# Performance work log

Measured on AMD Instinct MI355X. Metric: run time of the kernel, lower is better.

The kernel has to match this reference:

```python
import jax, jax.numpy as jnp
import numpy as np

B, S, E = 8, 1024, 512
H = 8            # num_heads
D = E // H       # head_dim
FFN = 2048
WINDOW = 5       # local_window_size
EPS = 1e-5


def _mha(x, in_w, in_b, out_w, out_b, mask=None):
    """PyTorch nn.MultiheadAttention (batch_first) forward. mask: True = blocked."""
    b, s, e = x.shape
    qkv = x @ in_w.T + in_b                      # [B,S,3E]
    q, k, v = jnp.split(qkv, 3, axis=-1)
    def heads(t):
        return t.reshape(b, s, H, D).transpose(0, 2, 1, 3)  # [B,H,S,D]
    q, k, v = heads(q), heads(k), heads(v)
    scores = jnp.einsum('bhsd,bhtd->bhst', q, k) / np.sqrt(D).astype(x.dtype)
    if mask is not None:
        scores = jnp.where(mask[None, None], -jnp.inf, scores)
    attn = jax.nn.softmax(scores, axis=-1)
    out = jnp.einsum('bhst,bhtd->bhsd', attn, v)  # [B,H,S,D]
    out = out.transpose(0, 2, 1, 3).reshape(b, s, e)
    return out @ out_w.T + out_b


def _layernorm(x, g, b):
    mu = jnp.mean(x, axis=-1, keepdims=True)
    var = jnp.mean(jnp.square(x - mu), axis=-1, keepdims=True)
    return (x - mu) * jax.lax.rsqrt(var + EPS) * g + b


def setup_inputs() -> dict:
    key = jax.random.key(0)
    ks = jax.random.split(key, 8)
    w = 0.02  # weight scale for numerical sanity
    return {
        'x': jax.random.normal(ks[0], (B, S, E), jnp.float32),
        'l_in_w': jax.random.normal(ks[1], (3 * E, E), jnp.float32) * w,
        'l_in_b': jnp.zeros((3 * E,), jnp.float32),
        'l_out_w': jax.random.normal(ks[2], (E, E), jnp.float32) * w,
        'l_out_b': jnp.zeros((E,), jnp.float32),
        'g_in_w': jax.random.normal(ks[3], (3 * E, E), jnp.float32) * w,
        'g_in_b': jnp.zeros((3 * E,), jnp.float32),
        'g_out_w': jax.random.normal(ks[4], (E, E), jnp.float32) * w,
        'g_out_b': jnp.zeros((E,), jnp.float32),
        'ffn_w1': jax.random.normal(ks[5], (FFN, E), jnp.float32) * w,
        'ffn_b1': jnp.zeros((FFN,), jnp.float32),
        'ffn_w2': jax.random.normal(ks[6], (E, FFN), jnp.float32) * w,
        'ffn_b2': jnp.zeros((E,), jnp.float32),
        'ln1_g': jnp.ones((E,), jnp.float32),
        'ln1_b': jnp.zeros((E,), jnp.float32),
        'ln2_g': jnp.ones((E,), jnp.float32),
        'ln2_b': jnp.zeros((E,), jnp.float32),
    }


def reference(x, l_in_w, l_in_b, l_out_w, l_out_b,
              g_in_w, g_in_b, g_out_w, g_out_b,
              ffn_w1, ffn_b1, ffn_w2, ffn_b2,
              ln1_g, ln1_b, ln2_g, ln2_b):
    s = x.shape[1]
    idx = jnp.arange(s)
    local_mask = jnp.abs(idx[:, None] - idx[None, :]) > WINDOW  # True = blocked
    local_out = _mha(x, l_in_w, l_in_b, l_out_w, l_out_b, mask=local_mask)
    global_out = _mha(x, g_in_w, g_in_b, g_out_w, g_out_b)
    x = x + local_out + global_out
    x = _layernorm(x, ln1_g, ln1_b)
    ffn = jax.nn.relu(x @ ffn_w1.T + ffn_b1) @ ffn_w2.T + ffn_b2
    x = _layernorm(x + ffn, ln2_g, ln2_b)
    return x
```

## Files before the change

### kernel.cpp

```cpp
#include <hip/hip_runtime.h>
#include <hip/hip_bf16.h>
#include <stdint.h>

#define Bb 8
#define Ss 1024
#define Ee 512
#define Hh 8
#define Dh 64
#define FFNd 2048
#define EPSv 1e-5f
#define QS 3072
#define OS 1024

typedef float f32x4 __attribute__((ext_vector_type(4)));
typedef int   i32x4 __attribute__((ext_vector_type(4)));

__device__ inline float bf2f(ushort u) {
    uint32_t x = ((uint32_t)u) << 16; float f; __builtin_memcpy(&f, &x, 4); return f;
}
__device__ inline ushort f2bf(float f) {
    uint32_t x; __builtin_memcpy(&x, &f, 4);
    uint32_t r = (x + 0x7FFFu + ((x >> 16) & 1u)) >> 16; return (ushort)r;
}

__device__ inline void gload16(const ushort* g, ushort* l) {
    __builtin_amdgcn_global_load_lds((const __attribute__((address_space(1))) void*)g,
                                     (__attribute__((address_space(3))) void*)l,
                                     16, 0, 0);
}

__device__ inline int vswz(int d, int kv) {
    return (d * 64 + kv) ^ ((((d & 7) ^ ((d >> 3) & 7)) & 7) << 3);
}

__device__ inline void cvt4_to(const float* src, int f, ushort* dst) {
    float4 v = *(const float4*)(src + f);
    ushort4 o;
    o.x = f2bf(v.x); o.y = f2bf(v.y); o.z = f2bf(v.z); o.w = f2bf(v.w);
    *(ushort4*)dst = o;
}
__global__ __launch_bounds__(256) void cvt_all(const float* __restrict__ s0, const float* __restrict__ s1,
                                               const float* __restrict__ s2, const float* __restrict__ s3,
                                               const float* __restrict__ s4, const float* __restrict__ s5,
                                               const float* __restrict__ s6,
                                               ushort* __restrict__ dx, ushort* __restrict__ dw) {
    int bid = blockIdx.x, tid = threadIdx.x;
    if (bid < 4096)      { int f = bid * 1024 + tid * 4;          cvt4_to(s0, f, dx + f); }
    else if (bid < 4864) { int f = (bid - 4096) * 1024 + tid * 4; cvt4_to(s1, f, dw + f); }
    else if (bid < 5632) { int f = (bid - 4864) * 1024 + tid * 4; cvt4_to(s2, f, dw + 786432 + f); }
    else if (bid < 5888) { int f = (bid - 5632) * 1024 + tid * 4; int n = f >> 9, k = f & 511;
                           cvt4_to(s3, f, dw + 1572864 + n * 1024 + k); }
    else if (bid < 6144) { int f = (bid - 5888) * 1024 + tid * 4; int n = f >> 9, k = f & 511;
                           cvt4_to(s4, f, dw + 1572864 + n * 1024 + 512 + k); }
    else if (bid < 7168) { int f = (bid - 6144) * 1024 + tid * 4; cvt4_to(s5, f, dw + 2097152 + f); }
    else                 { int f = (bid - 7168) * 1024 + tid * 4; cvt4_to(s6, f, dw + 3145728 + f); }
}

template<bool OUT_BF16, bool RELU>
__global__ __launch_bounds__(256) void gemm_bt(const ushort* __restrict__ A,
                                               const ushort* __restrict__ Bm,
                                               const float* __restrict__ bias,
                                               const float* __restrict__ bias2, int nb1,
                                               void* __restrict__ C,
                                               int M, int N, int K) {
    __shared__ ushort Alds[128 * 32];
    __shared__ ushort Blds[128 * 32];
    int tid  = threadIdx.x;
    int lane = tid & 63, w = tid >> 6;
    int wr = w >> 1, wc = w & 1;
    int g  = lane >> 4, fr = lane & 15;
    int m0 = blockIdx.y * 128, n0 = blockIdx.x * 128;

    int lr4 = lane >> 2;
    int lc8 = (lane & 3) * 8;
    const ushort* gA0 = A  + (size_t)(m0 + (w * 2) * 16 + lr4) * K + lc8;
    const ushort* gA1 = gA0 + (size_t)16 * K;
    const ushort* gB0 = Bm + (size_t)(n0 + (w * 2) * 16 + lr4) * K + lc8;
    const ushort* gB1 = gB0 + (size_t)16 * K;
    ushort* lA0 = Alds + (w * 2) * 16 * 32;
    ushort* lA1 = lA0 + 16 * 32;
    ushort* lB0 = Blds + (w * 2) * 16 * 32;
    ushort* lB1 = lB0 + 16 * 32;

    f32x4 acc[4][4] = {};

    for (int kb = 0; kb < K; kb += 32) {
        __syncthreads();
        gload16(gA0 + kb, lA0);
        gload16(gA1 + kb, lA1);
        gload16(gB0 + kb, lB0);
        gload16(gB1 + kb, lB1);
        __syncthreads();
        i32x4 af[4], bfr[4];
        #pragma unroll
        for (int mt = 0; mt < 4; ++mt)
            af[mt] = *(const i32x4*)(Alds + (wr * 64 + mt * 16 + fr) * 32 + g * 8);
        #pragma unroll
        for (int nt = 0; nt < 4; ++nt)
            bfr[nt] = *(const i32x4*)(Blds + (wc * 64 + nt * 16 + fr) * 32 + g * 8);
        #pragma unroll
        for (int mt = 0; mt < 4; ++mt)
            #pragma unroll
            for (int nt = 0; nt < 4; ++nt)
                asm("v_mfma_f32_16x16x32_bf16 %0, %1, %2, %0"
                    : "+v"(acc[mt][nt]) : "v"(af[mt]), "v"(bfr[nt]));
    }

    #pragma unroll
    for (int mt = 0; mt < 4; ++mt) {
        int r0 = m0 + wr * 64 + mt * 16 + g * 4;
        #pragma unroll
        for (int nt = 0; nt < 4; ++nt) {
            int c = n0 + wc * 64 + nt * 16 + fr;
            float bv = c < nb1 ? bias[c] : bias2[c - nb1];
            #pragma unroll
            for (int r = 0; r < 4; ++r) {
                float v = acc[mt][nt][r] + bv;
                if (RELU) v = v > 0.f ? v : 0.f;
                if (OUT_BF16) ((ushort*)C)[(size_t)(r0 + r) * N + c] = f2bf(v);
                else          ((float*)C)[(size_t)(r0 + r) * N + c] = v;
            }
        }
    }
}

template<bool SUMB>
__global__ __launch_bounds__(256) void gemm64(const ushort* __restrict__ A,
                                              const ushort* __restrict__ Bm,
                                              const float* __restrict__ bias,
                                              const float* __restrict__ bias2,
                                              float* __restrict__ C,
                                              int M, int N, int K) {
    __shared__ ushort Alds[64 * 32];
    __shared__ ushort Blds[128 * 32];
    int tid  = threadIdx.x;
    int lane = tid & 63, w = tid >> 6;
    int g  = lane >> 4, fr = lane & 15;
    int m0 = blockIdx.y * 64, n0 = blockIdx.x * 128;

    int lr4 = lane >> 2;
    int lc8 = (lane & 3) * 8;
    const ushort* gA  = A  + (size_t)(m0 + w * 16 + lr4) * K + lc8;
    const ushort* gB0 = Bm + (size_t)(n0 + w * 32 + lr4) * K + lc8;
    const ushort* gB1 = gB0 + (size_t)16 * K;
    ushort* lA  = Alds + w * 16 * 32;
    ushort* lB0 = Blds + w * 32 * 32;
    ushort* lB1 = lB0 + 16 * 32;

    f32x4 acc[4][2] = {};

    for (int kb = 0; kb < K; kb += 32) {
        __syncthreads();
        gload16(gA + kb, lA);
        gload16(gB0 + kb, lB0);
        gload16(gB1 + kb, lB1);
        __syncthreads();
        i32x4 af[4], bfr[2];
        #pragma unroll
        for (int mt = 0; mt < 4; ++mt)
            af[mt] = *(const i32x4*)(Alds + (mt * 16 + fr) * 32 + g * 8);
        #pragma unroll
        for (int nt = 0; nt < 2; ++nt)
            bfr[nt] = *(const i32x4*)(Blds + (w * 32 + nt * 16 + fr) * 32 + g * 8);
        #pragma unroll
        for (int mt = 0; mt < 4; ++mt)
            #pragma unroll
            for (int nt = 0; nt < 2; ++nt)
                asm("v_mfma_f32_16x16x32_bf16 %0, %1, %2, %0"
                    : "+v"(acc[mt][nt]) : "v"(af[mt]), "v"(bfr[nt]));
    }

    #pragma unroll
    for (int mt = 0; mt < 4; ++mt) {
        int r0 = m0 + mt * 16 + g * 4;
        #pragma unroll
        for (int nt = 0; nt < 2; ++nt) {
            int c = n0 + w * 32 + nt * 16 + fr;
            float bv = SUMB ? bias[c] + bias2[c] : bias[c];
            #pragma unroll
            for (int r = 0; r < 4; ++r)
                C[(size_t)(r0 + r) * N + c] = acc[mt][nt][r] + bv;
        }
    }
}

__global__ __launch_bounds__(256) void attn_global_mfma(const ushort* __restrict__ qkv,
                                                        ushort* __restrict__ out) {
    __shared__ ushort Klds[64 * 64];
    __shared__ ushort Vtlds[64 * 64];
    __shared__ ushort Plds[4][32 * 64];
    int tid  = threadIdx.x;
    int lane = tid & 63, w = tid >> 6;
    int fr = lane & 15, g = lane >> 4;
    int qtile = blockIdx.x & 7;
    int bh = blockIdx.x >> 3;
    int h = bh & 7, b = bh >> 3;
    const ushort* qp    = qkv + (size_t)b * Ss * QS + h * Dh;
    const ushort* kbase = qp + Ee;
    const ushort* vbase = qp + 2 * Ee;

    i32x4 qf[2][2];
    int q0 = qtile * 128 + w * 32;
    #pragma unroll
    for (int mt = 0; mt < 2; ++mt)
        #pragma unroll
        for (int kb = 0; kb < 2; ++kb)
            qf[mt][kb] = *(const i32x4*)(qp + (size_t)(q0 + mt * 16 + fr) * QS + kb * 32 + g * 8);

    f32x4 oacc[2][4] = {};
    f32x4 lsum[2] = {};
    ushort* Pw = Plds[w];

    i32x4 kr[2], vr[2];
    auto load_tile = [&](int kv0) {
        #pragma unroll
        for (int u = 0; u < 2; ++u) {
            int c = tid + u * 256;
            int row = c >> 3, col8 = c & 7;
            kr[u] = *(const i32x4*)(kbase + (size_t)(kv0 + row) * QS + col8 * 8);
            vr[u] = *(const i32x4*)(vbase + (size_t)(kv0 + row) * QS + col8 * 8);
        }
    };
    load_tile(0);

    for (int kt = 0; kt < 16; ++kt) {
        __syncthreads();
        #pragma unroll
        for (int u = 0; u < 2; ++u) {
            int c = tid + u * 256;
            int row = c >> 3, col8 = c & 7;
            int kidx = (row * 64 + col8 * 8) ^ ((row & 7) << 3);
            *(i32x4*)(Klds + kidx) = kr[u];
            ushort tmp[8];
            *(i32x4*)tmp = vr[u];
            #pragma unroll
            for (int j = 0; j < 8; ++j)
                Vtlds[vswz(col8 * 8 + j, row)] = tmp[j];
        }
        __syncthreads();
        if (kt < 15) load_tile((kt + 1) * 64);

        f32x4 sacc[2][4] = {};
        i32x4 kf[4][2];
        #pragma unroll
        for (int nt = 0; nt < 4; ++nt) {
            int kvl = nt * 16 + fr;
            #pragma unroll
            for (int kb = 0; kb < 2; ++kb)
                kf[nt][kb] = *(const i32x4*)(Klds + ((kvl * 64 + kb * 32 + g * 8) ^ ((kvl & 7) << 3)));
        }
        #pragma unroll
        for (int mt = 0; mt < 2; ++mt)
            #pragma unroll
            for (int nt = 0; nt < 4; ++nt)
                #pragma unroll
                for (int kb = 0; kb < 2; ++kb)
                    asm("v_mfma_f32_16x16x32_bf16 %0, %1, %2, %0"
                        : "+v"(sacc[mt][nt]) : "v"(qf[mt][kb]), "v"(kf[nt][kb]));

        #pragma unroll
        for (int mt = 0; mt < 2; ++mt) {
            #pragma unroll
            for (int r = 0; r < 4; ++r) {
                int ql = mt * 16 + g * 4 + r;
                int sw = (ql & 7) << 3;
                float e0 = __expf(sacc[mt][0][r] * 0.125f);
                float e1 = __expf(sacc[mt][1][r] * 0.125f);
                float e2 = __expf(sacc[mt][2][r] * 0.125f);
                float e3 = __expf(sacc[mt][3][r] * 0.125f);
                Pw[(ql * 64 +  0 + fr) ^ sw] = f2bf(e0);
                Pw[(ql * 64 + 16 + fr) ^ sw] = f2bf(e1);
                Pw[(ql * 64 + 32 + fr) ^ sw] = f2bf(e2);
                Pw[(ql * 64 + 48 + fr) ^ sw] = f2bf(e3);
                lsum[mt][r] += (e0 + e1) + (e2 + e3);
            }
        }

        i32x4 pa[2][2], vf[4][2];
        #pragma unroll
        for (int mt = 0; mt < 2; ++mt) {
            int ql = mt * 16 + fr;
            #pragma unroll
            for (int kb = 0; kb < 2; ++kb)
                pa[mt][kb] = *(const i32x4*)(Pw + ((ql * 64 + kb * 32 + g * 8) ^ ((ql & 7) << 3)));
        }
        #pragma unroll
        for (int dn = 0; dn < 4; ++dn) {
            int d = dn * 16 + fr;
            #pragma unroll
            for (int kb = 0; kb < 2; ++kb)
                vf[dn][kb] = *(const i32x4*)(Vtlds + vswz(d, kb * 32 + g * 8));
        }
        #pragma unroll
        for (int mt = 0; mt < 2; ++mt)
            #pragma unroll
            for (int dn = 0; dn < 4; ++dn)
                #pragma unroll
                for (int kb = 0; kb < 2; ++kb)
                    asm("v_mfma_f32_16x16x32_bf16 %0, %1, %2, %0"
                        : "+v"(oacc[mt][dn]) : "v"(pa[mt][kb]), "v"(vf[dn][kb]));
    }

    #pragma unroll
    for (int mt = 0; mt < 2; ++mt)
        #pragma unroll
        for (int r = 0; r < 4; ++r) {
            float s = lsum[mt][r];
            s += __shfl_xor(s, 1); s += __shfl_xor(s, 2);
            s += __shfl_xor(s, 4); s += __shfl_xor(s, 8);
            lsum[mt][r] = 1.f / s;
        }

    #pragma unroll
    for (int mt = 0; mt < 2; ++mt)
        #pragma unroll
        for (int r = 0; r < 4; ++r) {
            int qg = q0 + mt * 16 + g * 4 + r;
            size_t ob = (size_t)(b * Ss + qg) * OS + h * Dh;
            #pragma unroll
            for (int dn = 0; dn < 4; ++dn)
                out[ob + dn * 16 + fr] = f2bf(oacc[mt][dn][r] * lsum[mt][r]);
        }
}

__global__ __launch_bounds__(256) void attn_local_mfma(const ushort* __restrict__ qkv,
                                                       ushort* __restrict__ out) {
    __shared__ ushort Klds[64 * 64];
    __shared__ ushort Vtlds[64 * 64];
    __shared__ ushort Plds[4][32 * 64];
    int tid  = threadIdx.x;
    int lane = tid & 63, w = tid >> 6;
    int fr = lane & 15, g = lane >> 4;
    int qtile = blockIdx.x & 7;
    int bh = blockIdx.x >> 3;
    int h = bh & 7, b = bh >> 3;
    const ushort* qp    = qkv + (size_t)b * Ss * QS + h * Dh;
    const ushort* kbase = qp + Ee;
    const ushort* vbase = qp + 2 * Ee;

    i32x4 qf[2][2];
    int q0 = qtile * 128 + w * 32;
    #pragma unroll
    for (int mt = 0; mt < 2; ++mt)
        #pragma unroll
        for (int kb = 0; kb < 2; ++kb)
            qf[mt][kb] = *(const i32x4*)(qp + (size_t)(q0 + mt * 16 + fr) * QS + kb * 32 + g * 8);

    f32x4 oacc[2][4] = {};
    f32x4 lsum[2] = {};
    ushort* Pw = Plds[w];

    i32x4 kr[2], vr[2];
    auto load_tile = [&](int kv0) {
        #pragma unroll
        for (int u = 0; u < 2; ++u) {
            int c = tid + u * 256;
            int row = c >> 3, col8 = c & 7;
            kr[u] = *(const i32x4*)(kbase + (size_t)(kv0 + row) * QS + col8 * 8);
            vr[u] = *(const i32x4*)(vbase + (size_t)(kv0 + row) * QS + col8 * 8);
        }
    };

    int tq2 = qtile * 2;
    int kt0 = tq2 > 0 ? tq2 - 1 : 0;
    int kt1 = tq2 + 2 < 16 ? tq2 + 2 : 15;
    load_tile(kt0 * 64);

    for (int kt = kt0; kt <= kt1; ++kt) {
        int kv0 = kt * 64;
        __syncthreads();
        #pragma unroll
        for (int u = 0; u < 2; ++u) {
            int c = tid + u * 256;
            int row = c >> 3, col8 = c & 7;
            int kidx = (row * 64 + col8 * 8) ^ ((row & 7) << 3);
            *(i32x4*)(Klds + kidx) = kr[u];
            ushort tmp[8];
            *(i32x4*)tmp = vr[u];
            #pragma unroll
            for (int j = 0; j < 8; ++j)
                Vtlds[vswz(col8 * 8 + j, row)] = tmp[j];
        }
        __syncthreads();
        if (kt < kt1) load_tile((kt + 1) * 64);

        bool active = (kv0 <= q0 + 36) && (kv0 + 63 >= q0 - 5);
        if (active) {
            f32x4 sacc[2][4] = {};
            i32x4 kf[4][2];
            #pragma unroll
            for (int nt = 0; nt < 4; ++nt) {
                int kvl = nt * 16 + fr;
                #pragma unroll
                for (int kb = 0; kb < 2; ++kb)
                    kf[nt][kb] = *(const i32x4*)(Klds + ((kvl * 64 + kb * 32 + g * 8) ^ ((kvl & 7) << 3)));
            }
            #pragma unroll
            for (int mt = 0; mt < 2; ++mt)
                #pragma unroll
                for (int nt = 0; nt < 4; ++nt)
                    #pragma unroll
                    for (int kb = 0; kb < 2; ++kb)
                        asm("v_mfma_f32_16x16x32_bf16 %0, %1, %2, %0"
                            : "+v"(sacc[mt][nt]) : "v"(qf[mt][kb]), "v"(kf[nt][kb]));

            #pragma unroll
            for (int mt = 0; mt < 2; ++mt) {
                #pragma unroll
                for (int r = 0; r < 4; ++r) {
                    int ql = mt * 16 + g * 4 + r;
                    int sw = (ql & 7) << 3;
                    int d0 = (q0 + ql) - (kv0 + fr);
                    int d1 = d0 - 16, d2 = d0 - 32, d3 = d0 - 48;
                    float e0 = (d0 >= -5 && d0 <= 5) ? __expf(sacc[mt][0][r] * 0.125f) : 0.f;
                    float e1 = (d1 >= -5 && d1 <= 5) ? __expf(sacc[mt][1][r] * 0.125f) : 0.f;
                    float e2 = (d2 >= -5 && d2 <= 5) ? __expf(sacc[mt][2][r] * 0.125f) : 0.f;
                    float e3 = (d3 >= -5 && d3 <= 5) ? __expf(sacc[mt][3][r] * 0.125f) : 0.f;
                    Pw[(ql * 64 +  0 + fr) ^ sw] = f2bf(e0);
                    Pw[(ql * 64 + 16 + fr) ^ sw] = f2bf(e1);
                    Pw[(ql * 64 + 32 + fr) ^ sw] = f2bf(e2);
                    Pw[(ql * 64 + 48 + fr) ^ sw] = f2bf(e3);
                    lsum[mt][r] += (e0 + e1) + (e2 + e3);
                }
            }

            i32x4 pa[2][2], vf[4][2];
            #pragma unroll
            for (int mt = 0; mt < 2; ++mt) {
                int ql = mt * 16 + fr;
                #pragma unroll
                for (int kb = 0; kb < 2; ++kb)
                    pa[mt][kb] = *(const i32x4*)(Pw + ((ql * 64 + kb * 32 + g * 8) ^ ((ql & 7) << 3)));
            }
            #pragma unroll
            for (int dn = 0; dn < 4; ++dn) {
                int d = dn * 16 + fr;
                #pragma unroll
                for (int kb = 0; kb < 2; ++kb)
                    vf[dn][kb] = *(const i32x4*)(Vtlds + vswz(d, kb * 32 + g * 8));
            }
            #pragma unroll
            for (int mt = 0; mt < 2; ++mt)
                #pragma unroll
                for (int dn = 0; dn < 4; ++dn)
                    #pragma unroll
                    for (int kb = 0; kb < 2; ++kb)
                        asm("v_mfma_f32_16x16x32_bf16 %0, %1, %2, %0"
                            : "+v"(oacc[mt][dn]) : "v"(pa[mt][kb]), "v"(vf[dn][kb]));
        }
    }

    #pragma unroll
    for (int mt = 0; mt < 2; ++mt)
        #pragma unroll
        for (int r = 0; r < 4; ++r) {
            float s = lsum[mt][r];
            s += __shfl_xor(s, 1); s += __shfl_xor(s, 2);
            s += __shfl_xor(s, 4); s += __shfl_xor(s, 8);
            lsum[mt][r] = 1.f / s;
        }

    #pragma unroll
    for (int mt = 0; mt < 2; ++mt)
        #pragma unroll
        for (int r = 0; r < 4; ++r) {
            int qg = q0 + mt * 16 + g * 4 + r;
            size_t ob = (size_t)(b * Ss + qg) * OS + h * Dh;
            #pragma unroll
            for (int dn = 0; dn < 4; ++dn)
                out[ob + dn * 16 + fr] = f2bf(oacc[mt][dn][r] * lsum[mt][r]);
        }
}

__global__ __launch_bounds__(256) void ln_add2_dw(const float* __restrict__ x,
                                                  const float* __restrict__ p1,
                                                  const float* __restrict__ gam,
                                                  const float* __restrict__ bet,
                                                  ushort* __restrict__ yb,
                                                  float* __restrict__ yf) {
    int row  = blockIdx.x * 4 + (threadIdx.x >> 6);
    int lane = threadIdx.x & 63;
    size_t off = (size_t)row * Ee + lane * 8;
    float hv[8];
    float4 a0 = *(const float4*)(x + off),  a1 = *(const float4*)(x + off + 4);
    float4 b0 = *(const float4*)(p1 + off), b1 = *(const float4*)(p1 + off + 4);
    hv[0] = a0.x + b0.x; hv[1] = a0.y + b0.y; hv[2] = a0.z + b0.z; hv[3] = a0.w + b0.w;
    hv[4] = a1.x + b1.x; hv[5] = a1.y + b1.y; hv[6] = a1.z + b1.z; hv[7] = a1.w + b1.w;
    float s = 0.f;
    #pragma unroll
    for (int i = 0; i < 8; ++i) s += hv[i];
    #pragma unroll
    for (int o = 32; o; o >>= 1) s += __shfl_xor(s, o);
    float mu = s * (1.f / Ee);
    float vs = 0.f;
    #pragma unroll
    for (int i = 0; i < 8; ++i) { float d = hv[i] - mu; vs += d * d; }
    #pragma unroll
    for (int o = 32; o; o >>= 1) vs += __shfl_xor(vs, o);
    float rs = rsqrtf(vs * (1.f / Ee) + EPSv);
    #pragma unroll
    for (int i = 0; i < 8; ++i) {
        float yv = (hv[i] - mu) * rs * gam[lane * 8 + i] + bet[lane * 8 + i];
        yf[off + i] = yv;
        yb[off + i] = f2bf(yv);
    }
}

__global__ __launch_bounds__(256) void ln_add2(const float* __restrict__ a,
                                               const float* __restrict__ bsrc,
                                               const float* __restrict__ gam,
                                               const float* __restrict__ bet,
                                               float* __restrict__ outp) {
    int row  = blockIdx.x * 4 + (threadIdx.x >> 6);
    int lane = threadIdx.x & 63;
    size_t off = (size_t)row * Ee + lane * 8;
    float hv[8];
    float4 a0 = *(const float4*)(a + off),    a1 = *(const float4*)(a + off + 4);
    float4 b0 = *(const float4*)(bsrc + off), b1 = *(const float4*)(bsrc + off + 4);
    hv[0] = a0.x + b0.x; hv[1] = a0.y + b0.y; hv[2] = a0.z + b0.z; hv[3] = a0.w + b0.w;
    hv[4] = a1.x + b1.x; hv[5] = a1.y + b1.y; hv[6] = a1.z + b1.z; hv[7] = a1.w + b1.w;
    float s = 0.f;
    #pragma unroll
    for (int i = 0; i < 8; ++i) s += hv[i];
    #pragma unroll
    for (int o = 32; o; o >>= 1) s += __shfl_xor(s, o);
    float mu = s * (1.f / Ee);
    float vs = 0.f;
    #pragma unroll
    for (int i = 0; i < 8; ++i) { float d = hv[i] - mu; vs += d * d; }
    #pragma unroll
    for (int o = 32; o; o >>= 1) vs += __shfl_xor(vs, o);
    float rs = rsqrtf(vs * (1.f / Ee) + EPSv);
    #pragma unroll
    for (int i = 0; i < 8; ++i)
        outp[off + i] = (hv[i] - mu) * rs * gam[lane * 8 + i] + bet[lane * 8 + i];
}

extern "C" void kernel_launch(void* const* d_in, const int* in_sizes, int n_in,
                              void* d_out, int out_size, void* d_ws, size_t ws_size,
                              hipStream_t stream) {
    const float* x      = (const float*)d_in[0];
    const float* l_in_w = (const float*)d_in[1];
    const float* l_in_b = (const float*)d_in[2];
    const float* l_out_w= (const float*)d_in[3];
    const float* l_out_b= (const float*)d_in[4];
    const float* g_in_w = (const float*)d_in[5];
    const float* g_in_b = (const float*)d_in[6];
    const float* g_out_w= (const float*)d_in[7];
    const float* g_out_b= (const float*)d_in[8];
    const float* ffn_w1 = (const float*)d_in[9];
    const float* ffn_b1 = (const float*)d_in[10];
    const float* ffn_w2 = (const float*)d_in[11];
    const float* ffn_b2 = (const float*)d_in[12];
    const float* ln1_g  = (const float*)d_in[13];
    const float* ln1_b  = (const float*)d_in[14];
    const float* ln2_g  = (const float*)d_in[15];
    const float* ln2_b  = (const float*)d_in[16];

    char* ws = (char*)d_ws;
    ushort* xb       = (ushort*)(ws + 0);
    ushort* wb       = (ushort*)(ws + 8388608);
    ushort* w_cat    = wb + 1572864;
    ushort* w1b      = wb + 2097152;
    ushort* w2b      = wb + 3145728;
    ushort* qkvb     = (ushort*)(ws + 16777216);
    ushort* attnCat  = (ushort*)(ws + 67108864);
    float*  projM    = (float*)(ws + 16777216);
    ushort* y1b      = (ushort*)(ws + 50331648);
    float*  y1f      = (float*)(ws + 58720256);
    ushort* ffn1b    = (ushort*)(ws + 16777216);
    float*  ffn2f    = (float*)(ws + 75497472);

    const int M = Bb * Ss;

    cvt_all<<<dim3(8192), dim3(256), 0, stream>>>(x, l_in_w, g_in_w, l_out_w, g_out_w,
                                                  ffn_w1, ffn_w2, xb, wb);

    gemm_bt<true, false><<<dim3(24, 64), 256, 0, stream>>>(
        xb, wb, l_in_b, g_in_b, 1536, qkvb, M, QS, Ee);

    attn_local_mfma<<<dim3(Bb * Hh * (Ss / 128)), 256, 0, stream>>>(qkvb, attnCat);
    attn_global_mfma<<<dim3(Bb * Hh * (Ss / 128)), 256, 0, stream>>>(qkvb + 1536, attnCat + 512);

    gemm64<true><<<dim3(Ee / 128, M / 64), 256, 0, stream>>>(
        attnCat, w_cat, l_out_b, g_out_b, projM, M, Ee, 1024);

    ln_add2_dw<<<dim3(M / 4), 256, 0, stream>>>(x, projM, ln1_g, ln1_b, y1b, y1f);

    gemm_bt<true, true><<<dim3(16, 64), 256, 0, stream>>>(
        y1b, w1b, ffn_b1, ffn_b1, FFNd, ffn1b, M, FFNd, Ee);
    gemm64<false><<<dim3(Ee / 128, M / 64), 256, 0, stream>>>(
        ffn1b, w2b, ffn_b2, ffn_b2, ffn2f, M, Ee, FFNd);

    ln_add2<<<dim3(M / 4), 256, 0, stream>>>(y1f, ffn2f, ln2_g, ln2_b, (float*)d_out);
}
```

Measured before the change: 296.6 us.

## Double-buffer LDS tiles in both bf16 GEMM kernels to overlap loads with MFMA

Both GEMM kernels now keep two LDS buffers per operand. The next K-tile's global-to-LDS loads are issued before the MFMA work on the current tile, and there is one barrier per iteration instead of two. This is meant to hide global load latency behind matrix compute and to cut barrier overhead. In exchange, LDS usage per block doubles, which may reduce occupancy, and correctness relies on the barrier waiting for the in-flight loads.

Result: no change. 295.3 us (-0.4%).

```diff
diff --git a/kernel.cpp b/kernel.cpp
--- a/kernel.cpp
+++ b/kernel.cpp
@@ -63,8 +63,8 @@
                                                const float* __restrict__ bias2, int nb1,
                                                void* __restrict__ C,
                                                int M, int N, int K) {
-    __shared__ ushort Alds[128 * 32];
-    __shared__ ushort Blds[128 * 32];
+    __shared__ ushort Alds[2][128 * 32];
+    __shared__ ushort Blds[2][128 * 32];
     int tid  = threadIdx.x;
     int lane = tid & 63, w = tid >> 6;
     int wr = w >> 1, wc = w & 1;
@@ -77,33 +77,40 @@
     const ushort* gA1 = gA0 + (size_t)16 * K;
     const ushort* gB0 = Bm + (size_t)(n0 + (w * 2) * 16 + lr4) * K + lc8;
     const ushort* gB1 = gB0 + (size_t)16 * K;
-    ushort* lA0 = Alds + (w * 2) * 16 * 32;
-    ushort* lA1 = lA0 + 16 * 32;
-    ushort* lB0 = Blds + (w * 2) * 16 * 32;
-    ushort* lB1 = lB0 + 16 * 32;
+    int offA0 = (w * 2) * 16 * 32;
+    int offA1 = offA0 + 16 * 32;
 
     f32x4 acc[4][4] = {};
-
-    for (int kb = 0; kb < K; kb += 32) {
-        __syncthreads();
-        gload16(gA0 + kb, lA0);
-        gload16(gA1 + kb, lA1);
-        gload16(gB0 + kb, lB0);
-        gload16(gB1 + kb, lB1);
-        __syncthreads();
+    const int nst = K >> 5;
+
+    auto stage = [&](int t) {
+        int kb = t << 5, bi = t & 1;
+        gload16(gA0 + kb, Alds[bi] + offA0);
+        gload16(gA1 + kb, Alds[bi] + offA1);
+        gload16(gB0 + kb, Blds[bi] + offA0);
+        gload16(gB1 + kb, Blds[bi] + offA1);
+    };
+
+    stage(0);
+    __syncthreads();
+
+    for (int t = 0; t < nst; ++t) {
+        if (t + 1 < nst) stage(t + 1);
+        int bi = t & 1;
         i32x4 af[4], bfr[4];
         #pragma unroll
         for (int mt = 0; mt < 4; ++mt)
-            af[mt] = *(const i32x4*)(Alds + (wr * 64 + mt * 16 + fr) * 32 + g * 8);
+            af[mt] = *(const i32x4*)(Alds[bi] + (wr * 64 + mt * 16 + fr) * 32 + g * 8);
         #pragma unroll
         for (int nt = 0; nt < 4; ++nt)
-            bfr[nt] = *(const i32x4*)(Blds + (wc * 64 + nt * 16 + fr) * 32 + g * 8);
+            bfr[nt] = *(const i32x4*)(Blds[bi] + (wc * 64 + nt * 16 + fr) * 32 + g * 8);
         #pragma unroll
         for (int mt = 0; mt < 4; ++mt)
             #pragma unroll
             for (int nt = 0; nt < 4; ++nt)
                 asm("v_mfma_f32_16x16x32_bf16 %0, %1, %2, %0"
                     : "+v"(acc[mt][nt]) : "v"(af[mt]), "v"(bfr[nt]));
+        __syncthreads();
     }
 
     #pragma unroll
@@ -131,8 +138,8 @@
                                               const float* __restrict__ bias2,
                                               float* __restrict__ C,
                                               int M, int N, int K) {
-    __shared__ ushort Alds[64 * 32];
-    __shared__ ushort Blds[128 * 32];
+    __shared__ ushort Alds[2][64 * 32];
+    __shared__ ushort Blds[2][128 * 32];
     int tid  = threadIdx.x;
     int lane = tid & 63, w = tid >> 6;
     int g  = lane >> 4, fr = lane & 15;
@@ -143,31 +150,40 @@
     const ushort* gA  = A  + (size_t)(m0 + w * 16 + lr4) * K + lc8;
     const ushort* gB0 = Bm + (size_t)(n0 + w * 32 + lr4) * K + lc8;
     const ushort* gB1 = gB0 + (size_t)16 * K;
-    ushort* lA  = Alds + w * 16 * 32;
-    ushort* lB0 = Blds + w * 32 * 32;
-    ushort* lB1 = lB0 + 16 * 32;
+    int offA  = w * 16 * 32;
+    int offB0 = w * 32 * 32;
+    int offB1 = offB0 + 16 * 32;
 
     f32x4 acc[4][2] = {};
-
-    for (int kb = 0; kb < K; kb += 32) {
-        __syncthreads();
-        gload16(gA + kb, lA);
-        gload16(gB0 + kb, lB0);
-        gload16(gB1 + kb, lB1);
-        __syncthreads();
+    const int nst = K >> 5;
+
+    auto stage = [&](int t) {
+        int kb = t << 5, bi = t & 1;
+        gload16(gA + kb, Alds[bi] + offA);
+        gload16(gB0 + kb, Blds[bi] + offB0);
+        gload16(gB1 + kb, Blds[bi] + offB1);
+    };
+
+    stage(0);
+    __syncthreads();
+
+    for (int t = 0; t < nst; ++t) {
+        if (t + 1 < nst) stage(t + 1);
+        int bi = t & 1;
         i32x4 af[4], bfr[2];
         #pragma unroll
         for (int mt = 0; mt < 4; ++mt)
-            af[mt] = *(const i32x4*)(Alds + (mt * 16 + fr) * 32 + g * 8);
+            af[mt] = *(const i32x4*)(Alds[bi] + (mt * 16 + fr) * 32 + g * 8);
         #pragma unroll
         for (int nt = 0; nt < 2; ++nt)
-            bfr[nt] = *(const i32x4*)(Blds + (w * 32 + nt * 16 + fr) * 32 + g * 8);
+            bfr[nt] = *(const i32x4*)(Blds[bi] + (w * 32 + nt * 16 + fr) * 32 + g * 8);
         #pragma unroll
         for (int mt = 0; mt < 4; ++mt)
             #pragma unroll
             for (int nt = 0; nt < 2; ++nt)
                 asm("v_mfma_f32_16x16x32_bf16 %0, %1, %2, %0"
                     : "+v"(acc[mt][nt]) : "v"(af[mt]), "v"(bfr[nt]));
+        __syncthreads();
     }
 
     #pragma unroll
```
